# Kernel optimization log

Hardware: AMD Instinct MI355X
Metric: run time of the kernel (lower is better)

## Reference

```python
import jax, jax.numpy as jnp
import numpy as np

SEQ_LEN = 1024
WINDOW = 32
NUM_HEADS = 16
BATCH = 8
DIM = 1024


def make_local_mask(seq_len=SEQ_LEN, window=WINDOW):
    # True = position is MASKED (disallowed), matching the torch bool attn_mask.
    # torch allows j in [i - window//2, i + window//2] inclusive.
    i = np.arange(seq_len)[:, None]
    j = np.arange(seq_len)[None, :]
    half = window // 2
    allowed = (j >= i - half) & (j <= i + half)
    return jnp.asarray(~allowed)


def setup_inputs() -> dict:
    key = jax.random.key(0)
    k_x, k_wi, k_wo = jax.random.split(key, 3)
    scale_in = 1.0 / np.sqrt(DIM)
    return {
        "x": jax.random.normal(k_x, (BATCH, SEQ_LEN, DIM), dtype=jnp.float32),
        "w_in": jax.random.normal(k_wi, (3 * DIM, DIM), dtype=jnp.float32) * scale_in,
        "b_in": jnp.zeros((3 * DIM,), dtype=jnp.float32),
        "w_out": jax.random.normal(k_wo, (DIM, DIM), dtype=jnp.float32) * scale_in,
        "b_out": jnp.zeros((DIM,), dtype=jnp.float32),
        "mask": make_local_mask(),
    }


def reference(x, w_in, b_in, w_out, b_out, mask):
    B, S, D = x.shape
    H = NUM_HEADS
    hd = D // H
    # fused in-projection (torch nn.MultiheadAttention self-attn path)
    qkv = x @ w_in.T + b_in                      # [B, S, 3D]
    q, k, v = jnp.split(qkv, 3, axis=-1)
    q = q.reshape(B, S, H, hd).transpose(0, 2, 1, 3)  # [B, H, S, hd]
    k = k.reshape(B, S, H, hd).transpose(0, 2, 1, 3)
    v = v.reshape(B, S, H, hd).transpose(0, 2, 1, 3)
    scores = jnp.einsum("bhqd,bhkd->bhqk", q, k) / jnp.sqrt(jnp.asarray(hd, x.dtype))
    neg = jnp.asarray(jnp.finfo(x.dtype).min, x.dtype)
    scores = jnp.where(mask[None, None, :, :], neg, scores)
    attn = jax.nn.softmax(scores, axis=-1)
    ctx = jnp.einsum("bhqk,bhkd->bhqd", attn, v)  # [B, H, S, hd]
    ctx = ctx.transpose(0, 2, 1, 3).reshape(B, S, D)
    return ctx @ w_out.T + b_out
```

## Files before the change

kernel.cpp:

```cpp
#include <hip/hip_runtime.h>

#define S_LEN   1024
#define NH      16
#define HD      64
#define BATCHN  8
#define DMODEL  1024
#define HALF_W  16

typedef __attribute__((ext_vector_type(8))) short bf16x8;
typedef __attribute__((ext_vector_type(4))) float f32x4;

__device__ __forceinline__ unsigned short f2bf(float f) {
  unsigned u = __builtin_bit_cast(unsigned, f);
  u += 0x7fffu + ((u >> 16) & 1u);
  return (unsigned short)(u >> 16);
}
__device__ __forceinline__ float bf2f(unsigned short h) {
  return __builtin_bit_cast(float, ((unsigned)h) << 16);
}

__device__ __forceinline__ void gload_lds16(const void* g, void* l) {
  __builtin_amdgcn_global_load_lds(
      (const __attribute__((address_space(1))) void*)g,
      (__attribute__((address_space(3))) void*)l, 16, 0, 0);
}

#define XT  2097152
#define WIT  786432
#define WOT  262144
__global__ __launch_bounds__(256) void cvt_all_kernel(
    const float* __restrict__ x, const float* __restrict__ wi,
    const float* __restrict__ wo,
    unsigned short* __restrict__ xb, unsigned short* __restrict__ wib,
    unsigned short* __restrict__ wob) {
  const int total = XT + WIT + WOT;
  for (int t = blockIdx.x * 256 + threadIdx.x; t < total; t += 2048 * 256) {
    const float* in; unsigned short* out; int i;
    if (t < XT)            { in = x;  out = xb;  i = t; }
    else if (t < XT + WIT) { in = wi; out = wib; i = t - XT; }
    else                   { in = wo; out = wob; i = t - XT - WIT; }
    float4 v = reinterpret_cast<const float4*>(in)[i];
    ushort4 o = make_ushort4(f2bf(v.x), f2bf(v.y), f2bf(v.z), f2bf(v.w));
    reinterpret_cast<ushort4*>(out)[i] = o;
  }
}

#define MFMA_BF16 __builtin_amdgcn_mfma_f32_16x16x32_bf16

__global__ __launch_bounds__(512, 2) void gemm_inproj_kernel(
    const unsigned short* __restrict__ A,
    const unsigned short* __restrict__ B,
    const float* __restrict__ bias,
    unsigned short* __restrict__ C) {
  __shared__ __align__(16) unsigned short lds[81920];

  const int tid  = threadIdx.x;
  const int lane = tid & 63;
  const int wid  = tid >> 6;
  const int wm   = wid >> 2;
  const int wn   = wid & 3;
  const int lgrp = lane >> 4;
  const int l15  = lane & 15;

  const int sid = (blockIdx.x & 7) * 32 + (blockIdx.x >> 3);
  const int tileM = (sid >> 3) * 256;
  const int tileN = (sid & 7) * 384;

  const int srow = tid >> 2;
  const int scol = ((tid & 3) ^ ((tid >> 3) & 3)) * 8;
  const unsigned short* gA_s = A + (size_t)(tileM + srow) * 1024 + scol;
  const unsigned short* gB_s = B + (size_t)(tileN + srow) * 1024 + scol;

  const int fch  = (lgrp ^ ((l15 >> 1) & 3)) * 8;
  const int arow = (wm * 128 + l15) * 32 + fch;
  const int brow = (wn * 96 + l15) * 32 + fch;

  f32x4 acc[48] = {};

#define STG(S) do { const int _q = (S) & 3;                                \
    const unsigned short* _ga = gA_s + (S) * 32;                           \
    const unsigned short* _gb = gB_s + (S) * 32;                           \
    gload_lds16(_ga,          &lds[_q * 8192 + tid * 8]);                  \
    gload_lds16(_ga + 131072, &lds[_q * 8192 + 4096 + tid * 8]);           \
    gload_lds16(_gb,          &lds[32768 + _q * 12288 + tid * 8]);         \
    gload_lds16(_gb + 131072, &lds[32768 + _q * 12288 + 4096 + tid * 8]);  \
    gload_lds16(_gb + 262144, &lds[32768 + _q * 12288 + 8192 + tid * 8]);  \
  } while (0)

#define M24(MB)                                                            \
    acc[(MB+0)*6+0] = MFMA_BF16(a0_, b0_, acc[(MB+0)*6+0], 0, 0, 0);       \
    acc[(MB+0)*6+1] = MFMA_BF16(a0_, b1_, acc[(MB+0)*6+1], 0, 0, 0);       \
    acc[(MB+0)*6+2] = MFMA_BF16(a0_, b2_, acc[(MB+0)*6+2], 0, 0, 0);       \
    acc[(MB+0)*6+3] = MFMA_BF16(a0_, b3_, acc[(MB+0)*6+3], 0, 0, 0);       \
    acc[(MB+0)*6+4] = MFMA_BF16(a0_, b4_, acc[(MB+0)*6+4], 0, 0, 0);       \
    acc[(MB+0)*6+5] = MFMA_BF16(a0_, b5_, acc[(MB+0)*6+5], 0, 0, 0);       \
    acc[(MB+1)*6+0] = MFMA_BF16(a1_, b0_, acc[(MB+1)*6+0], 0, 0, 0);       \
    acc[(MB+1)*6+1] = MFMA_BF16(a1_, b1_, acc[(MB+1)*6+1], 0, 0, 0);       \
    acc[(MB+1)*6+2] = MFMA_BF16(a1_, b2_, acc[(MB+1)*6+2], 0, 0, 0);       \
    acc[(MB+1)*6+3] = MFMA_BF16(a1_, b3_, acc[(MB+1)*6+3], 0, 0, 0);       \
    acc[(MB+1)*6+4] = MFMA_BF16(a1_, b4_, acc[(MB+1)*6+4], 0, 0, 0);       \
    acc[(MB+1)*6+5] = MFMA_BF16(a1_, b5_, acc[(MB+1)*6+5], 0, 0, 0);       \
    acc[(MB+2)*6+0] = MFMA_BF16(a2_, b0_, acc[(MB+2)*6+0], 0, 0, 0);       \
    acc[(MB+2)*6+1] = MFMA_BF16(a2_, b1_, acc[(MB+2)*6+1], 0, 0, 0);       \
    acc[(MB+2)*6+2] = MFMA_BF16(a2_, b2_, acc[(MB+2)*6+2], 0, 0, 0);       \
    acc[(MB+2)*6+3] = MFMA_BF16(a2_, b3_, acc[(MB+2)*6+3], 0, 0, 0);       \
    acc[(MB+2)*6+4] = MFMA_BF16(a2_, b4_, acc[(MB+2)*6+4], 0, 0, 0);       \
    acc[(MB+2)*6+5] = MFMA_BF16(a2_, b5_, acc[(MB+2)*6+5], 0, 0, 0);       \
    acc[(MB+3)*6+0] = MFMA_BF16(a3_, b0_, acc[(MB+3)*6+0], 0, 0, 0);       \
    acc[(MB+3)*6+1] = MFMA_BF16(a3_, b1_, acc[(MB+3)*6+1], 0, 0, 0);       \
    acc[(MB+3)*6+2] = MFMA_BF16(a3_, b2_, acc[(MB+3)*6+2], 0, 0, 0);       \
    acc[(MB+3)*6+3] = MFMA_BF16(a3_, b3_, acc[(MB+3)*6+3], 0, 0, 0);       \
    acc[(MB+3)*6+4] = MFMA_BF16(a3_, b4_, acc[(MB+3)*6+4], 0, 0, 0);       \
    acc[(MB+3)*6+5] = MFMA_BF16(a3_, b5_, acc[(MB+3)*6+5], 0, 0, 0);

  STG(0); STG(1); STG(2);

#pragma unroll 1
  for (int p = 0; p < 32; ++p) {
    if (p < 30)       { asm volatile("s_waitcnt vmcnt(10)" ::: "memory"); }
    else if (p == 30) { asm volatile("s_waitcnt vmcnt(5)"  ::: "memory"); }
    else              { asm volatile("s_waitcnt vmcnt(0)"  ::: "memory"); }
    __builtin_amdgcn_sched_barrier(0);
    __builtin_amdgcn_s_barrier();

    if (p <= 28) STG(p + 3);

    const int slot = p & 3;
    const unsigned short* pa = &lds[slot * 8192 + arow];
    const unsigned short* pb = &lds[32768 + slot * 12288 + brow];

    bf16x8 b0_ = *(const bf16x8*)(pb);
    bf16x8 b1_ = *(const bf16x8*)(pb + 512);
    bf16x8 b2_ = *(const bf16x8*)(pb + 1024);
    bf16x8 b3_ = *(const bf16x8*)(pb + 1536);
    bf16x8 b4_ = *(const bf16x8*)(pb + 2048);
    bf16x8 b5_ = *(const bf16x8*)(pb + 2560);
    bf16x8 a0_ = *(const bf16x8*)(pa);
    bf16x8 a1_ = *(const bf16x8*)(pa + 512);
    bf16x8 a2_ = *(const bf16x8*)(pa + 1024);
    bf16x8 a3_ = *(const bf16x8*)(pa + 1536);
    asm volatile("s_waitcnt lgkmcnt(0)" ::: "memory");
    __builtin_amdgcn_sched_barrier(0);
    __builtin_amdgcn_s_setprio(1);
    M24(0)
    __builtin_amdgcn_s_setprio(0);

    a0_ = *(const bf16x8*)(pa + 2048);
    a1_ = *(const bf16x8*)(pa + 2560);
    a2_ = *(const bf16x8*)(pa + 3072);
    a3_ = *(const bf16x8*)(pa + 3584);
    asm volatile("s_waitcnt lgkmcnt(0)" ::: "memory");
    __builtin_amdgcn_sched_barrier(0);
    __builtin_amdgcn_s_setprio(1);
    M24(4)
    __builtin_amdgcn_s_setprio(0);
  }
#undef STG
#undef M24

#pragma unroll
  for (int nt = 0; nt < 6; ++nt) {
    const int col = tileN + wn * 96 + nt * 16 + l15;
    const float bs = bias[col];
#pragma unroll
    for (int mt = 0; mt < 8; ++mt) {
      const int row0 = tileM + wm * 128 + mt * 16 + lgrp * 4;
#pragma unroll
      for (int rr = 0; rr < 4; ++rr)
        C[(size_t)(row0 + rr) * 3072 + col] = f2bf(acc[mt * 6 + nt][rr] + bs);
    }
  }
}

__global__ __launch_bounds__(512, 2) void gemm_outproj_kernel(
    const unsigned short* __restrict__ A,
    const unsigned short* __restrict__ B,
    const float* __restrict__ bias,
    float* __restrict__ Cv) {
  __shared__ __align__(16) unsigned short lds[73728];

  const int tid  = threadIdx.x;
  const int lane = tid & 63;
  const int wid  = tid >> 6;
  const int wm   = wid >> 2;
  const int wn   = wid & 3;
  const int lgrp = lane >> 4;
  const int l15  = lane & 15;

  const int sid = (blockIdx.x & 7) * 32 + (blockIdx.x >> 3);
  const int tileM = (sid >> 2) * 128;
  const int tileN = (sid & 3) * 256;

  const int srow = tid >> 2;
  const int scol = ((tid & 3) ^ ((tid >> 3) & 3)) * 8;
  const unsigned short* gA_s = A + (size_t)(tileM + srow) * 1024 + scol;
  const unsigned short* gB_s = B + (size_t)(tileN + srow) * 1024 + scol;

  const int fch  = (lgrp ^ ((l15 >> 1) & 3)) * 8;
  const int arow = (wm * 64 + l15) * 32 + fch;
  const int brow = (wn * 64 + l15) * 32 + fch;

  f32x4 acc[4][4] = {};

#define STG(T) do { const int _q = (T) % 3;                                \
    const unsigned short* _ga = gA_s + (T) * 64;                           \
    const unsigned short* _gb = gB_s + (T) * 64;                           \
    gload_lds16(_ga,               &lds[_q * 24576 + tid * 8]);            \
    gload_lds16(_ga + 32,          &lds[_q * 24576 + 4096 + tid * 8]);     \
    gload_lds16(_gb,               &lds[_q * 24576 + 8192 + tid * 8]);     \
    gload_lds16(_gb + 131072,      &lds[_q * 24576 + 12288 + tid * 8]);    \
    gload_lds16(_gb + 32,          &lds[_q * 24576 + 16384 + tid * 8]);    \
    gload_lds16(_gb + 131072 + 32, &lds[_q * 24576 + 20480 + tid * 8]);    \
  } while (0)

#define SUB16(KH) do {                                                     \
    const unsigned short* _pa = &lds[slotb + (KH) * 4096 + arow];          \
    const unsigned short* _pb = &lds[slotb + 8192 + (KH) * 8192 + brow];   \
    bf16x8 a0_ = *(const bf16x8*)(_pa);                                    \
    bf16x8 a1_ = *(const bf16x8*)(_pa + 512);                              \
    bf16x8 a2_ = *(const bf16x8*)(_pa + 1024);                             \
    bf16x8 a3_ = *(const bf16x8*)(_pa + 1536);                             \
    bf16x8 nb0 = *(const bf16x8*)(_pb);                                    \
    bf16x8 nb1 = *(const bf16x8*)(_pb + 512);                              \
    bf16x8 nb2 = *(const bf16x8*)(_pb + 1024);                             \
    bf16x8 nb3 = *(const bf16x8*)(_pb + 1536);                             \
    asm volatile("s_waitcnt lgkmcnt(0)" ::: "memory");                     \
    __builtin_amdgcn_sched_barrier(0);                                     \
    __builtin_amdgcn_s_setprio(1);                                         \
    acc[0][0] = MFMA_BF16(a0_, nb0, acc[0][0], 0, 0, 0);                   \
    acc[0][1] = MFMA_BF16(a0_, nb1, acc[0][1], 0, 0, 0);                   \
    acc[0][2] = MFMA_BF16(a0_, nb2, acc[0][2], 0, 0, 0);                   \
    acc[0][3] = MFMA_BF16(a0_, nb3, acc[0][3], 0, 0, 0);                   \
    acc[1][0] = MFMA_BF16(a1_, nb0, acc[1][0], 0, 0, 0);                   \
    acc[1][1] = MFMA_BF16(a1_, nb1, acc[1][1], 0, 0, 0);                   \
    acc[1][2] = MFMA_BF16(a1_, nb2, acc[1][2], 0, 0, 0);                   \
    acc[1][3] = MFMA_BF16(a1_, nb3, acc[1][3], 0, 0, 0);                   \
    acc[2][0] = MFMA_BF16(a2_, nb0, acc[2][0], 0, 0, 0);                   \
    acc[2][1] = MFMA_BF16(a2_, nb1, acc[2][1], 0, 0, 0);                   \
    acc[2][2] = MFMA_BF16(a2_, nb2, acc[2][2], 0, 0, 0);                   \
    acc[2][3] = MFMA_BF16(a2_, nb3, acc[2][3], 0, 0, 0);                   \
    acc[3][0] = MFMA_BF16(a3_, nb0, acc[3][0], 0, 0, 0);                   \
    acc[3][1] = MFMA_BF16(a3_, nb1, acc[3][1], 0, 0, 0);                   \
    acc[3][2] = MFMA_BF16(a3_, nb2, acc[3][2], 0, 0, 0);                   \
    acc[3][3] = MFMA_BF16(a3_, nb3, acc[3][3], 0, 0, 0);                   \
    __builtin_amdgcn_s_setprio(0);                                         \
  } while (0)

  STG(0); STG(1);

#pragma unroll 1
  for (int p = 0; p < 16; ++p) {
    if (p < 15) { asm volatile("s_waitcnt vmcnt(6)" ::: "memory"); }
    else        { asm volatile("s_waitcnt vmcnt(0)" ::: "memory"); }
    __builtin_amdgcn_sched_barrier(0);
    __builtin_amdgcn_s_barrier();

    if (p <= 13) STG(p + 2);

    const int slotb = (p % 3) * 24576;
    SUB16(0);
    SUB16(1);
  }
#undef STG
#undef SUB16

#pragma unroll
  for (int nt = 0; nt < 4; ++nt) {
    const int col = tileN + wn * 64 + nt * 16 + l15;
    const float bs = bias[col];
#pragma unroll
    for (int mt = 0; mt < 4; ++mt) {
      const int row0 = tileM + wm * 64 + mt * 16 + lgrp * 4;
#pragma unroll
      for (int rr = 0; rr < 4; ++rr)
        Cv[(size_t)(row0 + rr) * 1024 + col] = acc[mt][nt][rr] + bs;
    }
  }
}

#define KST 72
#define PST 104

__global__ __launch_bounds__(256) void attn_local_kernel(
    const unsigned short* __restrict__ qkv, unsigned short* __restrict__ ctx) {
  __shared__ __align__(16) unsigned short sKP[96 * KST];
  __shared__ __align__(16) unsigned short sQ[64 * KST];
  __shared__ __align__(16) unsigned short sVT[64 * PST];

  const int tid  = threadIdx.x;
  const int lane = tid & 63;
  const int wid  = tid >> 6;
  const int qc   = lane & 15;
  const int lgrp = lane >> 4;

  const int qb = blockIdx.x & 15;
  const int h  = (blockIdx.x >> 4) & 15;
  const int b  = blockIdx.x >> 8;
  const int i0 = qb * 64;

  const unsigned short* hb = qkv + (size_t)b * S_LEN * 3072 + (size_t)h * HD;

#pragma unroll
  for (int it = 0; it < 3; ++it) {
    int c  = it * 256 + tid;
    int r  = c >> 3;
    int d0 = (c & 7) * 8;
    int j  = i0 - 16 + r;
    bf16x8 kv = {}, vv = {};
    if (0 <= j && j < S_LEN) {
      const unsigned short* rp = hb + (size_t)j * 3072;
      kv = *reinterpret_cast<const bf16x8*>(rp + DMODEL + d0);
      vv = *reinterpret_cast<const bf16x8*>(rp + 2 * DMODEL + d0);
    }
    *reinterpret_cast<bf16x8*>(&sKP[r * KST + d0]) = kv;
#pragma unroll
    for (int jj = 0; jj < 8; ++jj) {
      int dd = (jj + c) & 7;
      sVT[(d0 + dd) * PST + r] = (unsigned short)vv[dd];
    }
  }
#pragma unroll
  for (int it = 0; it < 2; ++it) {
    int c  = it * 256 + tid;
    int r  = c >> 3;
    int d0 = (c & 7) * 8;
    bf16x8 qv = *reinterpret_cast<const bf16x8*>(hb + (size_t)(i0 + r) * 3072 + d0);
    *reinterpret_cast<bf16x8*>(&sQ[r * KST + d0]) = qv;
  }
  __syncthreads();

  const int q0 = wid * 16;

  bf16x8 bq[2];
#pragma unroll
  for (int ks = 0; ks < 2; ++ks)
    bq[ks] = *reinterpret_cast<const bf16x8*>(
        &sQ[(q0 + qc) * KST + ks * 32 + lgrp * 8]);

  f32x4 st[6] = {};
#pragma unroll
  for (int kt = 0; kt < 6; ++kt) {
#pragma unroll
    for (int ks = 0; ks < 2; ++ks) {
      bf16x8 fa = *reinterpret_cast<const bf16x8*>(
          &sKP[(kt * 16 + qc) * KST + ks * 32 + lgrp * 8]);
      st[kt] = __builtin_amdgcn_mfma_f32_16x16x32_bf16(fa, bq[ks], st[kt], 0, 0, 0);
    }
  }
  __syncthreads();

  const int q = q0 + qc;
  float pv[6][4];
  float mx = -3.0e38f;
#pragma unroll
  for (int kt = 0; kt < 6; ++kt)
#pragma unroll
    for (int rr = 0; rr < 4; ++rr) {
      int kk = kt * 16 + lgrp * 4 + rr;
      int j  = i0 - 16 + kk;
      bool ok = (j >= 0) && (j < S_LEN) && (kk >= q) && (kk <= q + 32);
      float s = ok ? st[kt][rr] * 0.125f : -3.0e38f;
      pv[kt][rr] = s;
      mx = fmaxf(mx, s);
    }
  mx = fmaxf(mx, __shfl_xor(mx, 16, 64));
  mx = fmaxf(mx, __shfl_xor(mx, 32, 64));

  float rsum = 0.f;
#pragma unroll
  for (int kt = 0; kt < 6; ++kt)
#pragma unroll
    for (int rr = 0; rr < 4; ++rr) {
      float p = __expf(pv[kt][rr] - mx);
      pv[kt][rr] = p;
      rsum += p;
    }
  rsum += __shfl_xor(rsum, 16, 64);
  rsum += __shfl_xor(rsum, 32, 64);
  const float inv = 1.0f / rsum;

  unsigned short* sP = sKP;
#pragma unroll
  for (int kt = 0; kt < 6; ++kt) {
    ushort4 w = make_ushort4(f2bf(pv[kt][0]), f2bf(pv[kt][1]),
                             f2bf(pv[kt][2]), f2bf(pv[kt][3]));
    *reinterpret_cast<ushort4*>(&sP[(q0 + qc) * PST + kt * 16 + lgrp * 4]) = w;
  }

  bf16x8 pb[3];
#pragma unroll
  for (int ks = 0; ks < 3; ++ks)
    pb[ks] = *reinterpret_cast<const bf16x8*>(
        &sP[(q0 + qc) * PST + ks * 32 + lgrp * 8]);

  f32x4 ct[4] = {};
#pragma unroll
  for (int dt = 0; dt < 4; ++dt)
#pragma unroll
    for (int ks = 0; ks < 3; ++ks) {
      bf16x8 fa = *reinterpret_cast<const bf16x8*>(
          &sVT[(dt * 16 + qc) * PST + ks * 32 + lgrp * 8]);
      ct[dt] = __builtin_amdgcn_mfma_f32_16x16x32_bf16(fa, pb[ks], ct[dt], 0, 0, 0);
    }

  unsigned short* op =
      ctx + ((size_t)b * S_LEN + i0 + q0 + qc) * DMODEL + h * HD;
#pragma unroll
  for (int dt = 0; dt < 4; ++dt) {
    ushort4 w = make_ushort4(
        f2bf(ct[dt][0] * inv), f2bf(ct[dt][1] * inv),
        f2bf(ct[dt][2] * inv), f2bf(ct[dt][3] * inv));
    *reinterpret_cast<ushort4*>(op + dt * 16 + lgrp * 4) = w;
  }
}

extern "C" void kernel_launch(void* const* d_in, const int* in_sizes, int n_in,
                              void* d_out, int out_size, void* d_ws, size_t ws_size,
                              hipStream_t stream) {
  const float* x     = (const float*)d_in[0];
  const float* w_in  = (const float*)d_in[1];
  const float* b_in  = (const float*)d_in[2];
  const float* w_out = (const float*)d_in[3];
  const float* b_out = (const float*)d_in[4];
  float* out = (float*)d_out;

  unsigned short* xb   = (unsigned short*)d_ws;
  unsigned short* wib  = xb  + (size_t)8192 * 1024;
  unsigned short* wob  = wib + (size_t)3072 * 1024;
  unsigned short* qkv  = wob + (size_t)1024 * 1024;
  unsigned short* ctxb = qkv + (size_t)8192 * 3072;

  cvt_all_kernel<<<2048, 256, 0, stream>>>(x, w_in, w_out, xb, wib, wob);

  gemm_inproj_kernel<<<256, 512, 0, stream>>>(xb, wib, b_in, qkv);

  attn_local_kernel<<<BATCHN * NH * (S_LEN / 64), 256, 0, stream>>>(qkv, ctxb);

  gemm_outproj_kernel<<<256, 512, 0, stream>>>(ctxb, wob, b_out, out);
}
```

Before: 113.3 us.

## Shrink in-projection GEMM tile to 128x256 with 4 waves and triple buffering

The in-projection GEMM moves from 256x384 tiles computed by 512-thread blocks (256 blocks) to 128x256 tiles computed by 256-thread blocks (768 blocks). Each wave now covers all 128 rows and 64 columns, and the LDS pipeline drops from four stages to three, which cuts LDS and register use. The goal is more blocks for load balance across the CUs and higher occupancy. In exchange, each block reuses less data per load, so global and LDS traffic per FLOP rises, and there is one fewer prefetch stage to hide latency.

Result: slower. 117.7 us (+3.9%).

```diff
diff --git a/kernel.cpp b/kernel.cpp
--- a/kernel.cpp
+++ b/kernel.cpp
@@ -47,24 +47,22 @@
 
 #define MFMA_BF16 __builtin_amdgcn_mfma_f32_16x16x32_bf16
 
-__global__ __launch_bounds__(512, 2) void gemm_inproj_kernel(
+__global__ __launch_bounds__(256, 2) void gemm_inproj_kernel(
     const unsigned short* __restrict__ A,
     const unsigned short* __restrict__ B,
     const float* __restrict__ bias,
     unsigned short* __restrict__ C) {
-  __shared__ __align__(16) unsigned short lds[81920];
+  __shared__ __align__(16) unsigned short lds[36864];
 
   const int tid  = threadIdx.x;
   const int lane = tid & 63;
-  const int wid  = tid >> 6;
-  const int wm   = wid >> 2;
-  const int wn   = wid & 3;
+  const int wv   = tid >> 6;
   const int lgrp = lane >> 4;
   const int l15  = lane & 15;
 
-  const int sid = (blockIdx.x & 7) * 32 + (blockIdx.x >> 3);
-  const int tileM = (sid >> 3) * 256;
-  const int tileN = (sid & 7) * 384;
+  const int sid = (blockIdx.x & 7) * 96 + (blockIdx.x >> 3);
+  const int tileM = (sid / 12) * 128;
+  const int tileN = (sid % 12) * 256;
 
   const int srow = tid >> 2;
   const int scol = ((tid & 3) ^ ((tid >> 3) & 3)) * 8;
@@ -72,69 +70,59 @@
   const unsigned short* gB_s = B + (size_t)(tileN + srow) * 1024 + scol;
 
   const int fch  = (lgrp ^ ((l15 >> 1) & 3)) * 8;
-  const int arow = (wm * 128 + l15) * 32 + fch;
-  const int brow = (wn * 96 + l15) * 32 + fch;
-
-  f32x4 acc[48] = {};
-
-#define STG(S) do { const int _q = (S) & 3;                                \
+  const int arow = l15 * 32 + fch;
+  const int brow = 4096 + (wv * 64 + l15) * 32 + fch;
+
+  f32x4 acc[32] = {};
+
+#define STG(S) do { const int _q = (S) % 3;                                \
     const unsigned short* _ga = gA_s + (S) * 32;                           \
     const unsigned short* _gb = gB_s + (S) * 32;                           \
-    gload_lds16(_ga,          &lds[_q * 8192 + tid * 8]);                  \
-    gload_lds16(_ga + 131072, &lds[_q * 8192 + 4096 + tid * 8]);           \
-    gload_lds16(_gb,          &lds[32768 + _q * 12288 + tid * 8]);         \
-    gload_lds16(_gb + 131072, &lds[32768 + _q * 12288 + 4096 + tid * 8]);  \
-    gload_lds16(_gb + 262144, &lds[32768 + _q * 12288 + 8192 + tid * 8]);  \
+    gload_lds16(_ga,          &lds[_q * 12288 + tid * 8]);                 \
+    gload_lds16(_ga + 65536,  &lds[_q * 12288 + 2048 + tid * 8]);          \
+    gload_lds16(_gb,          &lds[_q * 12288 + 4096 + tid * 8]);          \
+    gload_lds16(_gb + 65536,  &lds[_q * 12288 + 6144 + tid * 8]);          \
+    gload_lds16(_gb + 131072, &lds[_q * 12288 + 8192 + tid * 8]);          \
+    gload_lds16(_gb + 196608, &lds[_q * 12288 + 10240 + tid * 8]);         \
   } while (0)
 
-#define M24(MB)                                                            \
-    acc[(MB+0)*6+0] = MFMA_BF16(a0_, b0_, acc[(MB+0)*6+0], 0, 0, 0);       \
-    acc[(MB+0)*6+1] = MFMA_BF16(a0_, b1_, acc[(MB+0)*6+1], 0, 0, 0);       \
-    acc[(MB+0)*6+2] = MFMA_BF16(a0_, b2_, acc[(MB+0)*6+2], 0, 0, 0);       \
-    acc[(MB+0)*6+3] = MFMA_BF16(a0_, b3_, acc[(MB+0)*6+3], 0, 0, 0);       \
-    acc[(MB+0)*6+4] = MFMA_BF16(a0_, b4_, acc[(MB+0)*6+4], 0, 0, 0);       \
-    acc[(MB+0)*6+5] = MFMA_BF16(a0_, b5_, acc[(MB+0)*6+5], 0, 0, 0);       \
-    acc[(MB+1)*6+0] = MFMA_BF16(a1_, b0_, acc[(MB+1)*6+0], 0, 0, 0);       \
-    acc[(MB+1)*6+1] = MFMA_BF16(a1_, b1_, acc[(MB+1)*6+1], 0, 0, 0);       \
-    acc[(MB+1)*6+2] = MFMA_BF16(a1_, b2_, acc[(MB+1)*6+2], 0, 0, 0);       \
-    acc[(MB+1)*6+3] = MFMA_BF16(a1_, b3_, acc[(MB+1)*6+3], 0, 0, 0);       \
-    acc[(MB+1)*6+4] = MFMA_BF16(a1_, b4_, acc[(MB+1)*6+4], 0, 0, 0);       \
-    acc[(MB+1)*6+5] = MFMA_BF16(a1_, b5_, acc[(MB+1)*6+5], 0, 0, 0);       \
-    acc[(MB+2)*6+0] = MFMA_BF16(a2_, b0_, acc[(MB+2)*6+0], 0, 0, 0);       \
-    acc[(MB+2)*6+1] = MFMA_BF16(a2_, b1_, acc[(MB+2)*6+1], 0, 0, 0);       \
-    acc[(MB+2)*6+2] = MFMA_BF16(a2_, b2_, acc[(MB+2)*6+2], 0, 0, 0);       \
-    acc[(MB+2)*6+3] = MFMA_BF16(a2_, b3_, acc[(MB+2)*6+3], 0, 0, 0);       \
-    acc[(MB+2)*6+4] = MFMA_BF16(a2_, b4_, acc[(MB+2)*6+4], 0, 0, 0);       \
-    acc[(MB+2)*6+5] = MFMA_BF16(a2_, b5_, acc[(MB+2)*6+5], 0, 0, 0);       \
-    acc[(MB+3)*6+0] = MFMA_BF16(a3_, b0_, acc[(MB+3)*6+0], 0, 0, 0);       \
-    acc[(MB+3)*6+1] = MFMA_BF16(a3_, b1_, acc[(MB+3)*6+1], 0, 0, 0);       \
-    acc[(MB+3)*6+2] = MFMA_BF16(a3_, b2_, acc[(MB+3)*6+2], 0, 0, 0);       \
-    acc[(MB+3)*6+3] = MFMA_BF16(a3_, b3_, acc[(MB+3)*6+3], 0, 0, 0);       \
-    acc[(MB+3)*6+4] = MFMA_BF16(a3_, b4_, acc[(MB+3)*6+4], 0, 0, 0);       \
-    acc[(MB+3)*6+5] = MFMA_BF16(a3_, b5_, acc[(MB+3)*6+5], 0, 0, 0);
-
-  STG(0); STG(1); STG(2);
+#define M16(MB)                                                            \
+    acc[(MB+0)*4+0] = MFMA_BF16(a0_, b0_, acc[(MB+0)*4+0], 0, 0, 0);       \
+    acc[(MB+0)*4+1] = MFMA_BF16(a0_, b1_, acc[(MB+0)*4+1], 0, 0, 0);       \
+    acc[(MB+0)*4+2] = MFMA_BF16(a0_, b2_, acc[(MB+0)*4+2], 0, 0, 0);       \
+    acc[(MB+0)*4+3] = MFMA_BF16(a0_, b3_, acc[(MB+0)*4+3], 0, 0, 0);       \
+    acc[(MB+1)*4+0] = MFMA_BF16(a1_, b0_, acc[(MB+1)*4+0], 0, 0, 0);       \
+    acc[(MB+1)*4+1] = MFMA_BF16(a1_, b1_, acc[(MB+1)*4+1], 0, 0, 0);       \
+    acc[(MB+1)*4+2] = MFMA_BF16(a1_, b2_, acc[(MB+1)*4+2], 0, 0, 0);       \
+    acc[(MB+1)*4+3] = MFMA_BF16(a1_, b3_, acc[(MB+1)*4+3], 0, 0, 0);       \
+    acc[(MB+2)*4+0] = MFMA_BF16(a2_, b0_, acc[(MB+2)*4+0], 0, 0, 0);       \
+    acc[(MB+2)*4+1] = MFMA_BF16(a2_, b1_, acc[(MB+2)*4+1], 0, 0, 0);       \
+    acc[(MB+2)*4+2] = MFMA_BF16(a2_, b2_, acc[(MB+2)*4+2], 0, 0, 0);       \
+    acc[(MB+2)*4+3] = MFMA_BF16(a2_, b3_, acc[(MB+2)*4+3], 0, 0, 0);       \
+    acc[(MB+3)*4+0] = MFMA_BF16(a3_, b0_, acc[(MB+3)*4+0], 0, 0, 0);       \
+    acc[(MB+3)*4+1] = MFMA_BF16(a3_, b1_, acc[(MB+3)*4+1], 0, 0, 0);       \
+    acc[(MB+3)*4+2] = MFMA_BF16(a3_, b2_, acc[(MB+3)*4+2], 0, 0, 0);       \
+    acc[(MB+3)*4+3] = MFMA_BF16(a3_, b3_, acc[(MB+3)*4+3], 0, 0, 0);
+
+  STG(0); STG(1);
 
 #pragma unroll 1
   for (int p = 0; p < 32; ++p) {
-    if (p < 30)       { asm volatile("s_waitcnt vmcnt(10)" ::: "memory"); }
-    else if (p == 30) { asm volatile("s_waitcnt vmcnt(5)"  ::: "memory"); }
-    else              { asm volatile("s_waitcnt vmcnt(0)"  ::: "memory"); }
+    if (p < 31) { asm volatile("s_waitcnt vmcnt(6)" ::: "memory"); }
+    else        { asm volatile("s_waitcnt vmcnt(0)" ::: "memory"); }
     __builtin_amdgcn_sched_barrier(0);
     __builtin_amdgcn_s_barrier();
 
-    if (p <= 28) STG(p + 3);
-
-    const int slot = p & 3;
-    const unsigned short* pa = &lds[slot * 8192 + arow];
-    const unsigned short* pb = &lds[32768 + slot * 12288 + brow];
+    if (p <= 29) STG(p + 2);
+
+    const int slotb = (p % 3) * 12288;
+    const unsigned short* pa = &lds[slotb + arow];
+    const unsigned short* pb = &lds[slotb + brow];
 
     bf16x8 b0_ = *(const bf16x8*)(pb);
     bf16x8 b1_ = *(const bf16x8*)(pb + 512);
     bf16x8 b2_ = *(const bf16x8*)(pb + 1024);
     bf16x8 b3_ = *(const bf16x8*)(pb + 1536);
-    bf16x8 b4_ = *(const bf16x8*)(pb + 2048);
-    bf16x8 b5_ = *(const bf16x8*)(pb + 2560);
     bf16x8 a0_ = *(const bf16x8*)(pa);
     bf16x8 a1_ = *(const bf16x8*)(pa + 512);
     bf16x8 a2_ = *(const bf16x8*)(pa + 1024);
@@ -142,7 +130,7 @@
     asm volatile("s_waitcnt lgkmcnt(0)" ::: "memory");
     __builtin_amdgcn_sched_barrier(0);
     __builtin_amdgcn_s_setprio(1);
-    M24(0)
+    M16(0)
     __builtin_amdgcn_s_setprio(0);
 
     a0_ = *(const bf16x8*)(pa + 2048);
@@ -152,22 +140,22 @@
     asm volatile("s_waitcnt lgkmcnt(0)" ::: "memory");
     __builtin_amdgcn_sched_barrier(0);
     __builtin_amdgcn_s_setprio(1);
-    M24(4)
+    M16(4)
     __builtin_amdgcn_s_setprio(0);
   }
 #undef STG
-#undef M24
-
-#pragma unroll
-  for (int nt = 0; nt < 6; ++nt) {
-    const int col = tileN + wn * 96 + nt * 16 + l15;
+#undef M16
+
+#pragma unroll
+  for (int nt = 0; nt < 4; ++nt) {
+    const int col = tileN + wv * 64 + nt * 16 + l15;
     const float bs = bias[col];
 #pragma unroll
     for (int mt = 0; mt < 8; ++mt) {
-      const int row0 = tileM + wm * 128 + mt * 16 + lgrp * 4;
+      const int row0 = tileM + mt * 16 + lgrp * 4;
 #pragma unroll
       for (int rr = 0; rr < 4; ++rr)
-        C[(size_t)(row0 + rr) * 3072 + col] = f2bf(acc[mt * 6 + nt][rr] + bs);
+        C[(size_t)(row0 + rr) * 3072 + col] = f2bf(acc[mt * 4 + nt][rr] + bs);
     }
   }
 }
@@ -432,7 +420,7 @@
 
   cvt_all_kernel<<<2048, 256, 0, stream>>>(x, w_in, w_out, xb, wib, wob);
 
-  gemm_inproj_kernel<<<256, 512, 0, stream>>>(xb, wib, b_in, qkv);
+  gemm_inproj_kernel<<<768, 256, 0, stream>>>(xb, wib, b_in, qkv);
 
   attn_local_kernel<<<BATCHN * NH * (S_LEN / 64), 256, 0, stream>>>(qkv, ctxb);
 
```

## Switch QKV GEMM to double-buffered 64-wide K stages with fewer barriers

Applied to the files above, without the earlier changes.

The in-projection GEMM main loop drops its four-slot ring of 32-wide K tiles (prefetch distance three, 32 iterations) in favour of two buffers of 64-wide K tiles (16 iterations). Each iteration runs two K-halves of MFMA work and issues ten global-to-LDS loads for the next stage. The aim is to halve the number of workgroup barriers and waitcnt stalls while keeping the same LDS footprint. In exchange, the next tile is issued only one iteration ahead and fully drained with vmcnt(0), so global-load latency may be less well hidden.

Measured after the change: 113.7 us. No clear change (+0.4%).

```diff
diff --git a/kernel.cpp b/kernel.cpp
--- a/kernel.cpp
+++ b/kernel.cpp
@@ -77,14 +77,19 @@
 
   f32x4 acc[48] = {};
 
-#define STG(S) do { const int _q = (S) & 3;                                \
-    const unsigned short* _ga = gA_s + (S) * 32;                           \
-    const unsigned short* _gb = gB_s + (S) * 32;                           \
-    gload_lds16(_ga,          &lds[_q * 8192 + tid * 8]);                  \
-    gload_lds16(_ga + 131072, &lds[_q * 8192 + 4096 + tid * 8]);           \
-    gload_lds16(_gb,          &lds[32768 + _q * 12288 + tid * 8]);         \
-    gload_lds16(_gb + 131072, &lds[32768 + _q * 12288 + 4096 + tid * 8]);  \
-    gload_lds16(_gb + 262144, &lds[32768 + _q * 12288 + 8192 + tid * 8]);  \
+#define STG(T) do { const int _s = ((T) & 1) * 40960;                      \
+    const unsigned short* _ga = gA_s + (T) * 64;                           \
+    const unsigned short* _gb = gB_s + (T) * 64;                           \
+    gload_lds16(_ga,                &lds[_s + tid * 8]);                   \
+    gload_lds16(_ga + 131072,       &lds[_s + 4096 + tid * 8]);            \
+    gload_lds16(_ga + 32,           &lds[_s + 8192 + tid * 8]);            \
+    gload_lds16(_ga + 131072 + 32,  &lds[_s + 12288 + tid * 8]);           \
+    gload_lds16(_gb,                &lds[_s + 16384 + tid * 8]);           \
+    gload_lds16(_gb + 131072,       &lds[_s + 20480 + tid * 8]);           \
+    gload_lds16(_gb + 262144,       &lds[_s + 24576 + tid * 8]);           \
+    gload_lds16(_gb + 32,           &lds[_s + 28672 + tid * 8]);           \
+    gload_lds16(_gb + 131072 + 32,  &lds[_s + 32768 + tid * 8]);           \
+    gload_lds16(_gb + 262144 + 32,  &lds[_s + 36864 + tid * 8]);           \
   } while (0)
 
 #define M24(MB)                                                            \
@@ -113,50 +118,53 @@
     acc[(MB+3)*6+4] = MFMA_BF16(a3_, b4_, acc[(MB+3)*6+4], 0, 0, 0);       \
     acc[(MB+3)*6+5] = MFMA_BF16(a3_, b5_, acc[(MB+3)*6+5], 0, 0, 0);
 
-  STG(0); STG(1); STG(2);
+#define KHALF(PAB, PBB) do {                                               \
+    const unsigned short* pa = (PAB);                                      \
+    const unsigned short* pb = (PBB);                                      \
+    bf16x8 b0_ = *(const bf16x8*)(pb);                                     \
+    bf16x8 b1_ = *(const bf16x8*)(pb + 512);                               \
+    bf16x8 b2_ = *(const bf16x8*)(pb + 1024);                              \
+    bf16x8 b3_ = *(const bf16x8*)(pb + 1536);                              \
+    bf16x8 b4_ = *(const bf16x8*)(pb + 2048);                              \
+    bf16x8 b5_ = *(const bf16x8*)(pb + 2560);                              \
+    bf16x8 a0_ = *(const bf16x8*)(pa);                                     \
+    bf16x8 a1_ = *(const bf16x8*)(pa + 512);                               \
+    bf16x8 a2_ = *(const bf16x8*)(pa + 1024);                              \
+    bf16x8 a3_ = *(const bf16x8*)(pa + 1536);                              \
+    asm volatile("s_waitcnt lgkmcnt(0)" ::: "memory");                     \
+    __builtin_amdgcn_sched_barrier(0);                                     \
+    __builtin_amdgcn_s_setprio(1);                                         \
+    M24(0)                                                                 \
+    __builtin_amdgcn_s_setprio(0);                                         \
+    a0_ = *(const bf16x8*)(pa + 2048);                                     \
+    a1_ = *(const bf16x8*)(pa + 2560);                                     \
+    a2_ = *(const bf16x8*)(pa + 3072);                                     \
+    a3_ = *(const bf16x8*)(pa + 3584);                                     \
+    asm volatile("s_waitcnt lgkmcnt(0)" ::: "memory");                     \
+    __builtin_amdgcn_sched_barrier(0);                                     \
+    __builtin_amdgcn_s_setprio(1);                                         \
+    M24(4)                                                                 \
+    __builtin_amdgcn_s_setprio(0);                                         \
+  } while (0)
+
+  STG(0); STG(1);
 
 #pragma unroll 1
-  for (int p = 0; p < 32; ++p) {
-    if (p < 30)       { asm volatile("s_waitcnt vmcnt(10)" ::: "memory"); }
-    else if (p == 30) { asm volatile("s_waitcnt vmcnt(5)"  ::: "memory"); }
-    else              { asm volatile("s_waitcnt vmcnt(0)"  ::: "memory"); }
+  for (int p = 0; p < 16; ++p) {
+    if (p == 0) { asm volatile("s_waitcnt vmcnt(10)" ::: "memory"); }
+    else        { asm volatile("s_waitcnt vmcnt(0)"  ::: "memory"); }
     __builtin_amdgcn_sched_barrier(0);
     __builtin_amdgcn_s_barrier();
 
-    if (p <= 28) STG(p + 3);
-
-    const int slot = p & 3;
-    const unsigned short* pa = &lds[slot * 8192 + arow];
-    const unsigned short* pb = &lds[32768 + slot * 12288 + brow];
-
-    bf16x8 b0_ = *(const bf16x8*)(pb);
-    bf16x8 b1_ = *(const bf16x8*)(pb + 512);
-    bf16x8 b2_ = *(const bf16x8*)(pb + 1024);
-    bf16x8 b3_ = *(const bf16x8*)(pb + 1536);
-    bf16x8 b4_ = *(const bf16x8*)(pb + 2048);
-    bf16x8 b5_ = *(const bf16x8*)(pb + 2560);
-    bf16x8 a0_ = *(const bf16x8*)(pa);
-    bf16x8 a1_ = *(const bf16x8*)(pa + 512);
-    bf16x8 a2_ = *(const bf16x8*)(pa + 1024);
-    bf16x8 a3_ = *(const bf16x8*)(pa + 1536);
-    asm volatile("s_waitcnt lgkmcnt(0)" ::: "memory");
-    __builtin_amdgcn_sched_barrier(0);
-    __builtin_amdgcn_s_setprio(1);
-    M24(0)
-    __builtin_amdgcn_s_setprio(0);
-
-    a0_ = *(const bf16x8*)(pa + 2048);
-    a1_ = *(const bf16x8*)(pa + 2560);
-    a2_ = *(const bf16x8*)(pa + 3072);
-    a3_ = *(const bf16x8*)(pa + 3584);
-    asm volatile("s_waitcnt lgkmcnt(0)" ::: "memory");
-    __builtin_amdgcn_sched_barrier(0);
-    __builtin_amdgcn_s_setprio(1);
-    M24(4)
-    __builtin_amdgcn_s_setprio(0);
+    if (p >= 1 && p <= 14) STG(p + 1);
+
+    const int slotb = (p & 1) * 40960;
+    KHALF(&lds[slotb + arow],        &lds[slotb + 16384 + brow]);
+    KHALF(&lds[slotb + 8192 + arow], &lds[slotb + 28672 + brow]);
   }
 #undef STG
 #undef M24
+#undef KHALF
 
 #pragma unroll
   for (int nt = 0; nt < 6; ++nt) {
```
